# Optimization experiments

Measured on AMD Instinct MI355X. Metric: run time of the kernel, lower is better.

## Reference

```python
import jax, jax.numpy as jnp
import numpy as np

D_MODEL = 1024
D_HIDDEN = 4096
NUM_EXPERT = 2
TOP_K = 1
W_SCALE = 0.02  # keep expert pre-exp outputs small so exp() in combine stays finite
EPS = float(np.finfo(float).eps)


def setup_inputs() -> dict:
    key = jax.random.key(0)
    ks = jax.random.split(key, 6)
    x = jax.random.normal(ks[0], (4, 4096, D_MODEL), dtype=jnp.float32)
    Wg = jax.random.normal(ks[1], (D_MODEL, NUM_EXPERT), dtype=jnp.float32) * W_SCALE
    bg = jax.random.normal(ks[2], (NUM_EXPERT,), dtype=jnp.float32) * W_SCALE
    We = jax.random.normal(ks[3], (NUM_EXPERT, D_MODEL, D_HIDDEN), dtype=jnp.float32) * W_SCALE
    be = jax.random.normal(ks[4], (NUM_EXPERT, D_HIDDEN), dtype=jnp.float32) * W_SCALE
    return {"x": x, "Wg": Wg, "bg": bg, "We": We, "be": be}


def reference(x, Wg, bg, We, be):
    B, N, C = x.shape
    xt = x.reshape(-1, C)                               # [T, C]
    # NaiveGate: linear -> top-k -> softmax over top-k logits -> dense scatter
    logits = xt @ Wg + bg                               # [T, E]
    top_v, top_i = jax.lax.top_k(logits, TOP_K)         # [T, k]
    top_g = jax.nn.softmax(top_v, axis=-1)              # [T, k] (==1.0 when k=1)
    gates = jnp.sum(jax.nn.one_hot(top_i, NUM_EXPERT, dtype=logits.dtype) * top_g[..., None], axis=1)  # [T, E]
    # expert FFNs (dense over all tokens; gate==0 tokens contribute nothing in combine,
    # matching SparseDispatcher semantics exactly)
    eo = jnp.einsum('tc,ech->eth', xt, We) + be[:, None, :]   # [E, T, H]
    # combine: sum_e gate[t,e] * exp(expert_e(x_t)); zeros -> eps; then log
    combined = jnp.einsum('te,eth->th', gates, jnp.exp(eo))   # [T, H]
    combined = jnp.where(combined == 0, EPS, combined)
    return jnp.log(combined).reshape(B, N, D_HIDDEN)
```

## Files before the change

### kernel.cpp

```cpp
#include <hip/hip_runtime.h>
#include <hip/hip_bf16.h>


#define DM 1024
#define DH 4096
#define KS 32
#define NS (DM / KS)

typedef __attribute__((ext_vector_type(4))) float f32x4;
typedef __attribute__((ext_vector_type(8))) __bf16 bf16x8;

__device__ __forceinline__ unsigned short f2bf(float f) {
    union { float f; unsigned u; } a; a.f = f;
    unsigned u = a.u;
    u += 0x7fffu + ((u >> 16) & 1u);
    return (unsigned short)(u >> 16);
}

__device__ __forceinline__ void gl16(const unsigned short* g, unsigned short* l) {
    __builtin_amdgcn_global_load_lds(
        (const __attribute__((address_space(1))) unsigned int*)(g),
        (__attribute__((address_space(3))) unsigned int*)(l), 16, 0, 0);
}

__global__ __launch_bounds__(1024) void prep(
    const float* __restrict__ x, const float* __restrict__ Wg,
    const float* __restrict__ bg, const float* __restrict__ We, int T,
    unsigned short* __restrict__ xbf, unsigned short* __restrict__ webt,
    int* __restrict__ perm, int* __restrict__ eidx, int* __restrict__ cur)
{
    int bid = blockIdx.x, tid = threadIdx.x;

    if (bid < 512) {
        __shared__ unsigned short tile[4][64][72];
        int sub = tid >> 8, t2 = tid & 255;
        int g = bid * 4 + sub;
        int e = g >> 10, rr = g & 1023, kt = rr >> 6, ht = rr & 63;
        int k0 = kt * 64, h0 = ht * 64;
        int k = t2 >> 2, hc = t2 & 3;
        const float* src = We + ((size_t)e * DM + k0 + k) * DH + h0 + hc * 16;
#pragma unroll
        for (int j = 0; j < 4; ++j) {
            f32x4 v = *(const f32x4*)(src + j * 4);
#pragma unroll
            for (int q = 0; q < 4; ++q)
                tile[sub][hc * 16 + j * 4 + q][k] = f2bf(v[q]);
        }
        __syncthreads();
        int h = t2 >> 2, kc = t2 & 3;
        unsigned short* dst = webt + ((size_t)e * DH + h0 + h) * DM + k0 + kc * 16;
        *(uint4*)(dst)     = *(const uint4*)&tile[sub][h][kc * 16];
        *(uint4*)(dst + 8) = *(const uint4*)&tile[sub][h][kc * 16 + 8];
        return;
    }

    __shared__ unsigned char eL[64];
    int gb = bid - 512;
    int lane = tid & 63, w = tid >> 6;
    float wgv[32];
#pragma unroll
    for (int j = 0; j < 8; ++j)
        *(f32x4*)&wgv[j * 4] = *(const f32x4*)(Wg + lane * 32 + j * 4);
    float bg0 = bg[0], bg1 = bg[1];
    int t0 = gb * 64 + w * 4;
#pragma unroll
    for (int tl = 0; tl < 4; ++tl) {
        int t = t0 + tl;
        const float* xr = x + (size_t)t * DM + lane * 16;
        double g0 = 0.0, g1 = 0.0;
        unsigned hw[8];
#pragma unroll
        for (int j = 0; j < 4; ++j) {
            f32x4 v = *(const f32x4*)(xr + j * 4);
#pragma unroll
            for (int q = 0; q < 4; ++q) {
                g0 += (double)v[q] * (double)wgv[2 * (j * 4 + q)];
                g1 += (double)v[q] * (double)wgv[2 * (j * 4 + q) + 1];
            }
            hw[j * 2]     = (unsigned)f2bf(v[0]) | ((unsigned)f2bf(v[1]) << 16);
            hw[j * 2 + 1] = (unsigned)f2bf(v[2]) | ((unsigned)f2bf(v[3]) << 16);
        }
        unsigned short* xw = xbf + (size_t)t * DM + lane * 16;
        uint4 u0; u0.x = hw[0]; u0.y = hw[1]; u0.z = hw[2]; u0.w = hw[3];
        uint4 u1; u1.x = hw[4]; u1.y = hw[5]; u1.z = hw[6]; u1.w = hw[7];
        *(uint4*)(xw)     = u0;
        *(uint4*)(xw + 8) = u1;
#pragma unroll
        for (int off = 32; off; off >>= 1) {
            g0 += __shfl_xor(g0, off);
            g1 += __shfl_xor(g1, off);
        }
        if (lane == 0) {
            int ee = ((g1 + (double)bg1) > (g0 + (double)bg0)) ? 1 : 0;
            eidx[t] = ee;
            eL[w * 4 + tl] = (unsigned char)ee;
        }
    }
    __syncthreads();
    if (w == 0) {
        int myE = eL[lane];
        unsigned long long m1 = __ballot(myE != 0);
        int tot1 = __popcll(m1);
        int b0 = 0, b1 = 0;
        if (lane == 0) {
            b0 = atomicAdd(cur, 64 - tot1);
            b1 = atomicAdd(cur + 1, tot1);
        }
        b0 = __shfl(b0, 0);
        b1 = __shfl(b1, 0);
        unsigned long long lm = (1ull << lane) - 1ull;
        int rank = __popcll((myE ? m1 : ~m1) & lm);
        int dstp = myE ? (T - b1 - tot1 + rank) : (b0 + rank);
        perm[dstp] = gb * 64 + lane;
    }
}

__global__ __launch_bounds__(512, 2) void moe_gemm(
    const unsigned short* __restrict__ xbf,
    const unsigned short* __restrict__ webt,
    const float* __restrict__ be,
    const int* __restrict__ perm,
    const int* __restrict__ eidx,
    float* __restrict__ out)
{
    __shared__ unsigned short As[4][256 * KS];
    __shared__ unsigned short Bs[4][256 * KS];
    const int nwg = gridDim.x;
    const int bid = blockIdx.x;
    const int swz = (bid & 7) * (nwg >> 3) + (bid >> 3);
    const int mt = swz >> 4, nt = swz & 15;
    const int m0 = mt * 256, n0 = nt * 256;
    const int tid = threadIdx.x, lane = tid & 63, wid = tid >> 6;
    const int wm = wid >> 2, wn = wid & 3;

    const unsigned short* aptr[2];
    size_t bofs[2];
    unsigned lofs[2];
#pragma unroll
    for (int j = 0; j < 2; ++j) {
        int c = wid * 128 + j * 64 + lane;
        int row = c >> 2, k8 = (c & 3) ^ ((row >> 1) & 3);
        aptr[j] = xbf + (size_t)perm[m0 + row] * DM + k8 * 8;
        bofs[j] = (size_t)(n0 + row) * DM + k8 * 8;
        lofs[j] = (unsigned)(wid * 128 + j * 64) * 8;
    }

    const int rA = wm * 128 + (lane & 15);
    const int rB = wn * 64 + (lane & 15);
    const int offA = rA * KS + (((lane >> 4) ^ ((rA >> 1) & 3)) * 8);
    const int offB = rB * KS + (((lane >> 4) ^ ((rB >> 1) & 3)) * 8);

    const int e_lo = eidx[perm[m0]];
    const int e_hi = eidx[perm[m0 + 255]];

    for (int e = e_lo; e <= e_hi; ++e) {
        const unsigned short* wb = webt + (size_t)e * DH * DM;

#pragma unroll
        for (int s = 0; s < 3; ++s) {
#pragma unroll
            for (int j = 0; j < 2; ++j) gl16(aptr[j] + s * KS, As[s] + lofs[j]);
#pragma unroll
            for (int j = 0; j < 2; ++j) gl16(wb + bofs[j] + s * KS, Bs[s] + lofs[j]);
        }
        f32x4 acc[8][4];
#pragma unroll
        for (int mi = 0; mi < 8; ++mi)
#pragma unroll
            for (int ni = 0; ni < 4; ++ni) acc[mi][ni] = 0.f;
        asm volatile("s_waitcnt vmcnt(8)" ::: "memory");
        __builtin_amdgcn_s_barrier();

        bf16x8 bfr[4];
        auto phase = [&](int s, int mh, bool doStage, int wcnt) {
            const unsigned short* areg = As[s & 3];
            bf16x8 af[4];
            if (mh == 0) {
                const unsigned short* breg = Bs[s & 3];
#pragma unroll
                for (int ni = 0; ni < 4; ++ni)
                    bfr[ni] = *(const bf16x8*)(breg + offB + ni * 16 * KS);
#pragma unroll
                for (int mi = 0; mi < 4; ++mi)
                    af[mi] = *(const bf16x8*)(areg + offA + mi * 16 * KS);
            } else {
#pragma unroll
                for (int mi = 0; mi < 4; ++mi)
                    af[mi] = *(const bf16x8*)(areg + offA + (mi + 4) * 16 * KS);
            }
            if (doStage) {
                int t = s + 3;
                if (mh == 0) {
                    unsigned short* dreg = As[t & 3];
#pragma unroll
                    for (int j = 0; j < 2; ++j) gl16(aptr[j] + t * KS, dreg + lofs[j]);
                } else {
                    unsigned short* dreg = Bs[t & 3];
#pragma unroll
                    for (int j = 0; j < 2; ++j) gl16(wb + bofs[j] + t * KS, dreg + lofs[j]);
                }
            }
            __builtin_amdgcn_sched_barrier(0);
            __builtin_amdgcn_s_barrier();
            asm volatile("s_waitcnt lgkmcnt(0)" ::: "memory");
            __builtin_amdgcn_sched_barrier(0);
            __builtin_amdgcn_s_setprio(1);
            const int mb = mh * 4;
#pragma unroll
            for (int mi = 0; mi < 4; ++mi)
#pragma unroll
                for (int ni = 0; ni < 4; ++ni)
                    acc[mb + mi][ni] = __builtin_amdgcn_mfma_f32_16x16x32_bf16(
                        af[mi], bfr[ni], acc[mb + mi][ni], 0, 0, 0);
            __builtin_amdgcn_s_setprio(0);
            __builtin_amdgcn_sched_barrier(0);
            if (wcnt == 6)      asm volatile("s_waitcnt vmcnt(6)" ::: "memory");
            else if (wcnt == 4) asm volatile("s_waitcnt vmcnt(4)" ::: "memory");
            else if (wcnt == 0) asm volatile("s_waitcnt vmcnt(0)" ::: "memory");
            __builtin_amdgcn_s_barrier();
            __builtin_amdgcn_sched_barrier(0);
        };

#pragma unroll 1
        for (int it = 0; it < 7; ++it) {
            int sb = it * 4;
#pragma unroll
            for (int q = 0; q < 4; ++q) {
                phase(sb + q, 0, true, -1);
                phase(sb + q, 1, true, 6);
            }
        }
        phase(28, 0, true,  -1);
        phase(28, 1, true,   6);
        phase(29, 0, false, -1);
        phase(29, 1, false,  4);
        phase(30, 0, false, -1);
        phase(30, 1, false,  0);
        phase(31, 0, false, -1);
        phase(31, 1, false, -1);

        const int colc = n0 + wn * 64 + (lane & 15);
        float bev[4];
#pragma unroll
        for (int ni = 0; ni < 4; ++ni) bev[ni] = be[e * DH + colc + ni * 16];
        const int rb = m0 + wm * 128 + (lane >> 4) * 4;
#pragma unroll
        for (int mi = 0; mi < 8; ++mi) {
#pragma unroll
            for (int r = 0; r < 4; ++r) {
                int tk = perm[rb + mi * 16 + r];
                if (e_lo == e_hi || eidx[tk] == e) {
                    float* orow = out + (size_t)tk * DH + colc;
#pragma unroll
                    for (int ni = 0; ni < 4; ++ni)
                        orow[ni * 16] = acc[mi][ni][r] + bev[ni];
                }
            }
        }
    }
}

extern "C" void kernel_launch(void* const* d_in, const int* in_sizes, int n_in,
                              void* d_out, int out_size, void* d_ws, size_t ws_size,
                              hipStream_t stream) {
    const float* x  = (const float*)d_in[0];
    const float* Wg = (const float*)d_in[1];
    const float* bg = (const float*)d_in[2];
    const float* We = (const float*)d_in[3];
    const float* be = (const float*)d_in[4];
    float* out = (float*)d_out;
    int T = in_sizes[0] / DM;

    char* ws = (char*)d_ws;
    int* cur  = (int*)ws;
    int* perm = (int*)(ws + 4096);
    int* eidx = (int*)(ws + 4096 + 65536);
    unsigned short* webt = (unsigned short*)(ws + 4096 + 2 * 65536);
    unsigned short* xbf  = (unsigned short*)(ws + 4096 + 2 * 65536 + (size_t)2 * DH * DM * 2);

    hipMemsetAsync(cur, 0, 8, stream);
    hipLaunchKernelGGL(prep, dim3(512 + T / 64), dim3(1024), 0, stream,
                       x, Wg, bg, We, T, xbf, webt, perm, eidx, cur);
    int nblk = (T / 256) * (DH / 256);
    hipLaunchKernelGGL(moe_gemm, dim3(nblk), dim3(512), 0, stream,
                       xbf, webt, be, perm, eidx, out);
}
```

Baseline: 252.5 us.

## Shrink GEMM tiles to 128x128 with simple single-buffered loop and LDS-staged epilogue

Replaces the 256x256 tile, 512-thread kernel with its hand-scheduled 4-stage LDS pipeline by a 128x128 tile, 256-thread kernel that loads one K-slice per iteration between two barriers. The epilogue now goes through LDS so each lane writes contiguous 16-byte nontemporal stores instead of scattered scalar stores. The aim is more blocks and occupancy, and better-coalesced output writes. The cost is the loss of load/compute overlap and of per-tile data reuse, so more global traffic per FLOP.

```diff
diff --git a/kernel.cpp b/kernel.cpp
--- a/kernel.cpp
+++ b/kernel.cpp
@@ -115,7 +115,7 @@
     }
 }
 
-__global__ __launch_bounds__(512, 2) void moe_gemm(
+__global__ __launch_bounds__(256, 3) void moe_gemm(
     const unsigned short* __restrict__ xbf,
     const unsigned short* __restrict__ webt,
     const float* __restrict__ be,
@@ -123,138 +123,93 @@
     const int* __restrict__ eidx,
     float* __restrict__ out)
 {
-    __shared__ unsigned short As[4][256 * KS];
-    __shared__ unsigned short Bs[4][256 * KS];
+    __shared__ __align__(16) char smem[17408];
+    unsigned short* As = (unsigned short*)smem;
+    unsigned short* Bs = (unsigned short*)(smem + 8192);
+
     const int nwg = gridDim.x;
     const int bid = blockIdx.x;
     const int swz = (bid & 7) * (nwg >> 3) + (bid >> 3);
-    const int mt = swz >> 4, nt = swz & 15;
-    const int m0 = mt * 256, n0 = nt * 256;
+    const int mt = swz >> 5, nt = swz & 31;
+    const int m0 = mt * 128, n0 = nt * 128;
     const int tid = threadIdx.x, lane = tid & 63, wid = tid >> 6;
-    const int wm = wid >> 2, wn = wid & 3;
-
-    const unsigned short* aptr[2];
-    size_t bofs[2];
-    unsigned lofs[2];
-#pragma unroll
-    for (int j = 0; j < 2; ++j) {
-        int c = wid * 128 + j * 64 + lane;
-        int row = c >> 2, k8 = (c & 3) ^ ((row >> 1) & 3);
-        aptr[j] = xbf + (size_t)perm[m0 + row] * DM + k8 * 8;
-        bofs[j] = (size_t)(n0 + row) * DM + k8 * 8;
-        lofs[j] = (unsigned)(wid * 128 + j * 64) * 8;
-    }
-
-    const int rA = wm * 128 + (lane & 15);
+    const int wm = wid >> 1, wn = wid & 1;
+
+    const unsigned short *aptr0, *aptr1;
+    size_t bofs0, bofs1;
+    {
+        int c0 = tid, c1 = tid + 256;
+        int r0 = c0 >> 2, k80 = (c0 & 3) ^ ((r0 >> 1) & 3);
+        int r1 = c1 >> 2, k81 = (c1 & 3) ^ ((r1 >> 1) & 3);
+        aptr0 = xbf + (size_t)perm[m0 + r0] * DM + k80 * 8;
+        aptr1 = xbf + (size_t)perm[m0 + r1] * DM + k81 * 8;
+        bofs0 = (size_t)(n0 + r0) * DM + k80 * 8;
+        bofs1 = (size_t)(n0 + r1) * DM + k81 * 8;
+    }
+
+    const int rA = wm * 64 + (lane & 15);
     const int rB = wn * 64 + (lane & 15);
     const int offA = rA * KS + (((lane >> 4) ^ ((rA >> 1) & 3)) * 8);
     const int offB = rB * KS + (((lane >> 4) ^ ((rB >> 1) & 3)) * 8);
 
     const int e_lo = eidx[perm[m0]];
-    const int e_hi = eidx[perm[m0 + 255]];
+    const int e_hi = eidx[perm[m0 + 127]];
 
     for (int e = e_lo; e <= e_hi; ++e) {
         const unsigned short* wb = webt + (size_t)e * DH * DM;
 
-#pragma unroll
-        for (int s = 0; s < 3; ++s) {
-#pragma unroll
-            for (int j = 0; j < 2; ++j) gl16(aptr[j] + s * KS, As[s] + lofs[j]);
-#pragma unroll
-            for (int j = 0; j < 2; ++j) gl16(wb + bofs[j] + s * KS, Bs[s] + lofs[j]);
-        }
-        f32x4 acc[8][4];
-#pragma unroll
-        for (int mi = 0; mi < 8; ++mi)
+        f32x4 acc[4][4];
+#pragma unroll
+        for (int mi = 0; mi < 4; ++mi)
 #pragma unroll
             for (int ni = 0; ni < 4; ++ni) acc[mi][ni] = 0.f;
-        asm volatile("s_waitcnt vmcnt(8)" ::: "memory");
-        __builtin_amdgcn_s_barrier();
-
-        bf16x8 bfr[4];
-        auto phase = [&](int s, int mh, bool doStage, int wcnt) {
-            const unsigned short* areg = As[s & 3];
-            bf16x8 af[4];
-            if (mh == 0) {
-                const unsigned short* breg = Bs[s & 3];
+
+#pragma unroll 1
+        for (int kt = 0; kt < NS; ++kt) {
+            __syncthreads();
+            gl16(aptr0 + kt * KS, As + tid * 8);
+            gl16(aptr1 + kt * KS, As + (tid + 256) * 8);
+            gl16(wb + bofs0 + kt * KS, Bs + tid * 8);
+            gl16(wb + bofs1 + kt * KS, Bs + (tid + 256) * 8);
+            __syncthreads();
+
+            bf16x8 af[4], bfr[4];
+#pragma unroll
+            for (int mi = 0; mi < 4; ++mi) af[mi] = *(const bf16x8*)(As + offA + mi * 16 * KS);
+#pragma unroll
+            for (int ni = 0; ni < 4; ++ni) bfr[ni] = *(const bf16x8*)(Bs + offB + ni * 16 * KS);
+#pragma unroll
+            for (int mi = 0; mi < 4; ++mi)
 #pragma unroll
                 for (int ni = 0; ni < 4; ++ni)
-                    bfr[ni] = *(const bf16x8*)(breg + offB + ni * 16 * KS);
-#pragma unroll
-                for (int mi = 0; mi < 4; ++mi)
-                    af[mi] = *(const bf16x8*)(areg + offA + mi * 16 * KS);
-            } else {
-#pragma unroll
-                for (int mi = 0; mi < 4; ++mi)
-                    af[mi] = *(const bf16x8*)(areg + offA + (mi + 4) * 16 * KS);
-            }
-            if (doStage) {
-                int t = s + 3;
-                if (mh == 0) {
-                    unsigned short* dreg = As[t & 3];
-#pragma unroll
-                    for (int j = 0; j < 2; ++j) gl16(aptr[j] + t * KS, dreg + lofs[j]);
-                } else {
-                    unsigned short* dreg = Bs[t & 3];
-#pragma unroll
-                    for (int j = 0; j < 2; ++j) gl16(wb + bofs[j] + t * KS, dreg + lofs[j]);
-                }
-            }
-            __builtin_amdgcn_sched_barrier(0);
-            __builtin_amdgcn_s_barrier();
-            asm volatile("s_waitcnt lgkmcnt(0)" ::: "memory");
-            __builtin_amdgcn_sched_barrier(0);
-            __builtin_amdgcn_s_setprio(1);
-            const int mb = mh * 4;
-#pragma unroll
-            for (int mi = 0; mi < 4; ++mi)
-#pragma unroll
-                for (int ni = 0; ni < 4; ++ni)
-                    acc[mb + mi][ni] = __builtin_amdgcn_mfma_f32_16x16x32_bf16(
-                        af[mi], bfr[ni], acc[mb + mi][ni], 0, 0, 0);
-            __builtin_amdgcn_s_setprio(0);
-            __builtin_amdgcn_sched_barrier(0);
-            if (wcnt == 6)      asm volatile("s_waitcnt vmcnt(6)" ::: "memory");
-            else if (wcnt == 4) asm volatile("s_waitcnt vmcnt(4)" ::: "memory");
-            else if (wcnt == 0) asm volatile("s_waitcnt vmcnt(0)" ::: "memory");
-            __builtin_amdgcn_s_barrier();
-            __builtin_amdgcn_sched_barrier(0);
-        };
-
-#pragma unroll 1
-        for (int it = 0; it < 7; ++it) {
-            int sb = it * 4;
-#pragma unroll
-            for (int q = 0; q < 4; ++q) {
-                phase(sb + q, 0, true, -1);
-                phase(sb + q, 1, true, 6);
-            }
-        }
-        phase(28, 0, true,  -1);
-        phase(28, 1, true,   6);
-        phase(29, 0, false, -1);
-        phase(29, 1, false,  4);
-        phase(30, 0, false, -1);
-        phase(30, 1, false,  0);
-        phase(31, 0, false, -1);
-        phase(31, 1, false, -1);
-
-        const int colc = n0 + wn * 64 + (lane & 15);
+                    acc[mi][ni] = __builtin_amdgcn_mfma_f32_16x16x32_bf16(
+                        af[mi], bfr[ni], acc[mi][ni], 0, 0, 0);
+        }
+
+        __syncthreads();
+        float* ep = (float*)smem + wid * (16 * 68);
+        const int colb = n0 + wn * 64;
         float bev[4];
 #pragma unroll
-        for (int ni = 0; ni < 4; ++ni) bev[ni] = be[e * DH + colc + ni * 16];
-        const int rb = m0 + wm * 128 + (lane >> 4) * 4;
-#pragma unroll
-        for (int mi = 0; mi < 8; ++mi) {
-#pragma unroll
-            for (int r = 0; r < 4; ++r) {
-                int tk = perm[rb + mi * 16 + r];
-                if (e_lo == e_hi || eidx[tk] == e) {
-                    float* orow = out + (size_t)tk * DH + colc;
-#pragma unroll
-                    for (int ni = 0; ni < 4; ++ni)
-                        orow[ni * 16] = acc[mi][ni][r] + bev[ni];
-                }
+        for (int ni = 0; ni < 4; ++ni) bev[ni] = be[e * DH + colb + ni * 16 + (lane & 15)];
+        const bool multi = (e_lo != e_hi);
+        const int rowb = m0 + wm * 64;
+
+#pragma unroll
+        for (int mi = 0; mi < 4; ++mi) {
+#pragma unroll
+            for (int ni = 0; ni < 4; ++ni)
+#pragma unroll
+                for (int r = 0; r < 4; ++r)
+                    ep[((lane >> 4) * 4 + r) * 68 + ni * 16 + (lane & 15)] =
+                        acc[mi][ni][r] + bev[ni];
+#pragma unroll
+            for (int g = 0; g < 4; ++g) {
+                f32x4 v = *(const f32x4*)&ep[(g * 4 + (lane >> 4)) * 68 + (lane & 15) * 4];
+                int tk = perm[rowb + mi * 16 + g * 4 + (lane >> 4)];
+                if (!multi || eidx[tk] == e)
+                    __builtin_nontemporal_store(
+                        v, (f32x4*)(out + (size_t)tk * DH + colb + (lane & 15) * 4));
             }
         }
     }
@@ -281,7 +236,7 @@
     hipMemsetAsync(cur, 0, 8, stream);
     hipLaunchKernelGGL(prep, dim3(512 + T / 64), dim3(1024), 0, stream,
                        x, Wg, bg, We, T, xbf, webt, perm, eidx, cur);
-    int nblk = (T / 256) * (DH / 256);
-    hipLaunchKernelGGL(moe_gemm, dim3(nblk), dim3(512), 0, stream,
+    int nblk = (T / 128) * (DH / 128);
+    hipLaunchKernelGGL(moe_gemm, dim3(nblk), dim3(256), 0, stream,
                        xbf, webt, be, perm, eidx, out);
 }
```

Measured after the change: 223.7 us. -11.4%, faster.
